# Kernel tuning notes

Measured on AMD Instinct MI355X. Metric: run time of the kernel, lower is better.

## Reference

```python
import jax, jax.numpy as jnp
import numpy as np

DIM = 1024
NUM_HEADS = 16
HEAD_DIM = DIM // NUM_HEADS


def setup_inputs() -> dict:
    key = jax.random.key(0)
    k_x, k_qkv, k_proj, k_pb = jax.random.split(key, 4)
    B, N, C = 4, 2048, DIM
    x = jax.random.normal(k_x, (B, N, C), dtype=jnp.float32)
    # Dense 'qkv': kernel [C, 3C], no bias (qkv_bias=False)
    W_qkv = jax.random.normal(k_qkv, (C, 3 * C), dtype=jnp.float32) * (C ** -0.5)
    # Dense 'proj': kernel [C, C] + bias [C] (proj_bias=True)
    W_proj = jax.random.normal(k_proj, (C, C), dtype=jnp.float32) * (C ** -0.5)
    b_proj = jax.random.normal(k_pb, (C,), dtype=jnp.float32) * 0.01
    return {"x": x, "W_qkv": W_qkv, "W_proj": W_proj, "b_proj": b_proj}


def reference(x, W_qkv, W_proj, b_proj):
    B, N, C = x.shape
    H, D = NUM_HEADS, HEAD_DIM
    scale = D ** -0.5
    qkv = x @ W_qkv  # [B, N, 3C]
    qkv = qkv.reshape(B, N, 3, H, D).transpose(2, 0, 3, 1, 4)  # [3, B, H, N, D]
    q, k, v = qkv[0], qkv[1], qkv[2]
    attn = jnp.einsum('bhnd,bhmd->bhnm', q, k) * scale  # [B, H, N, N]
    attn = jax.nn.softmax(attn, axis=-1)
    out = jnp.einsum('bhnm,bhmd->bhnd', attn, v)  # [B, H, N, D]
    out = out.transpose(0, 2, 1, 3).reshape(B, N, C)
    return out @ W_proj + b_proj
```

## Files before the change

kernel.cpp:

```cpp
#include <hip/hip_runtime.h>
#include <hip/hip_bf16.h>
#include <cstdint>
#include <cstddef>

#define C_DIM 1024
#define N_HEADS 16
#define H_DIM 64
#define N_BATCH 4
#define SEQ_LEN 2048
#define N_BH 64
#define M_ROWS 8192

typedef __attribute__((ext_vector_type(8))) short bf16x8;
typedef __attribute__((ext_vector_type(4))) float f32x4;
typedef __attribute__((ext_vector_type(8))) float f32x8;
typedef __attribute__((ext_vector_type(2))) float f32x2;
typedef __attribute__((ext_vector_type(16))) float f32x16;
typedef __attribute__((ext_vector_type(4))) unsigned short us4;
typedef __attribute__((ext_vector_type(8))) unsigned short us8;
typedef __attribute__((ext_vector_type(4))) float fl4;

__device__ __forceinline__ unsigned short f2bf(float f) {
  union { float f; unsigned u; } v; v.f = f;
  unsigned r = (v.u + 0x7FFFu + ((v.u >> 16) & 1u)) >> 16;
  return (unsigned short)r;
}

__device__ __forceinline__ unsigned pk2(float a, float b) {
  union { __hip_bfloat162 h2; unsigned u; } c;
  c.h2 = __float22bfloat162_rn(float2{a, b});
  return c.u;
}

__device__ __forceinline__ void gload16(const void* g, void* l) {
  __builtin_amdgcn_global_load_lds(
      (const __attribute__((address_space(1))) unsigned int*)g,
      (__attribute__((address_space(3))) unsigned int*)l, 16, 0, 0);
}

__global__ void cast_x_kernel(const float* __restrict__ in,
                              unsigned short* __restrict__ out, int n8) {
  int i = blockIdx.x * blockDim.x + threadIdx.x;
  if (i >= n8) return;
  const fl4* p = reinterpret_cast<const fl4*>(in) + (size_t)i * 2;
  fl4 a = p[0], b = p[1];
  us8 w;
  w[0] = f2bf(a[0]); w[1] = f2bf(a[1]); w[2] = f2bf(a[2]); w[3] = f2bf(a[3]);
  w[4] = f2bf(b[0]); w[5] = f2bf(b[1]); w[6] = f2bf(b[2]); w[7] = f2bf(b[3]);
  *(reinterpret_cast<us8*>(out) + i) = w;
}

__global__ void transpose_cast_kernel(const float* __restrict__ in,
                                      unsigned short* __restrict__ out,
                                      int R, int C) {
  __shared__ float tile[64][65];
  int t = threadIdx.x;
  int tc = blockIdx.x * 64;
  int tr = blockIdx.y * 64;
  int hi = t >> 4, lo = t & 15;
#pragma unroll
  for (int i = 0; i < 4; ++i) {
    int r = i * 16 + hi;
    int c = lo * 4;
    fl4 v = *reinterpret_cast<const fl4*>(&in[(size_t)(tr + r) * C + tc + c]);
    tile[c + 0][r] = v[0]; tile[c + 1][r] = v[1];
    tile[c + 2][r] = v[2]; tile[c + 3][r] = v[3];
  }
  __syncthreads();
#pragma unroll
  for (int i = 0; i < 4; ++i) {
    int c = i * 16 + hi;
    int r = lo * 4;
    us4 w;
    w[0] = f2bf(tile[c][r + 0]); w[1] = f2bf(tile[c][r + 1]);
    w[2] = f2bf(tile[c][r + 2]); w[3] = f2bf(tile[c][r + 3]);
    *reinterpret_cast<us4*>(&out[(size_t)(tc + c) * R + tr + r]) = w;
  }
}

template <int EPI>
__global__ __launch_bounds__(256, 3) void gemm_v2_kernel(
    const unsigned short* __restrict__ A, const unsigned short* __restrict__ Bt,
    unsigned short* __restrict__ outQ, unsigned short* __restrict__ outK,
    unsigned short* __restrict__ outVt, float* __restrict__ outF,
    const float* __restrict__ bias, int K) {
  __shared__ __attribute__((aligned(16))) char lds[3 * 16384];
  const int tid = threadIdx.x;
  const int lane = tid & 63, wave = tid >> 6;
  const int wr = wave >> 1, wn = wave & 1;
  const int brow = blockIdx.y * 128;
  const int bcol = blockIdx.x * 128;
  const int rr = lane & 15, g = lane >> 4;

  const int rbase =
      (rr >> 1) * 128 + (((((rr & 1) << 2) | g) ^ (rr >> 1)) << 4);

  const int s1 = tid + 256;
  const int l0 = tid >> 3, v0 = (tid & 7) ^ (l0 & 7);
  const int l1 = s1 >> 3, v1 = (s1 & 7) ^ (l1 & 7);
  const int m0 = 2 * l0 + (v0 >> 2), g0 = v0 & 3;
  const int m1 = 2 * l1 + (v1 >> 2), g1 = v1 & 3;
  const char* srcA0 = (const char*)(A + (size_t)(brow + m0) * K + g0 * 8);
  const char* srcA1 = (const char*)(A + (size_t)(brow + m1) * K + g1 * 8);
  const char* srcB0 = (const char*)(Bt + (size_t)(bcol + m0) * K + g0 * 8);
  const char* srcB1 = (const char*)(Bt + (size_t)(bcol + m1) * K + g1 * 8);
  const int oA0 = wave * 1024 + (lane & 63) * 16;
  const int oA1 = oA0 + 4096;
  const int oB0 = oA0 + 8192;
  const int oB1 = oA0 + 12288;

  f32x4 acc[4][4];
#pragma unroll
  for (int m = 0; m < 4; ++m)
#pragma unroll
    for (int n = 0; n < 4; ++n) acc[m][n] = (f32x4){0.f, 0.f, 0.f, 0.f};

  const int NT = K >> 5;

#pragma unroll
  for (int pt = 0; pt < 2; ++pt) {
    char* bb = lds + pt * 16384;
    size_t ko = (size_t)pt * 64;
    gload16(srcA0 + ko, bb + oA0);
    gload16(srcA1 + ko, bb + oA1);
    gload16(srcB0 + ko, bb + oB0);
    gload16(srcB1 + ko, bb + oB1);
  }

  int rbuf = 0, nbuf = 2;
  for (int kt = 0; kt < NT; ++kt) {
    if (kt < NT - 1) {
      asm volatile("s_waitcnt vmcnt(4)" ::: "memory");
    } else {
      asm volatile("s_waitcnt vmcnt(0)" ::: "memory");
    }
    __builtin_amdgcn_sched_barrier(0);
    __builtin_amdgcn_s_barrier();
    __builtin_amdgcn_sched_barrier(0);
    if (kt + 2 < NT) {
      char* bb = lds + nbuf * 16384;
      size_t ko = (size_t)(kt + 2) * 64;
      gload16(srcA0 + ko, bb + oA0);
      gload16(srcA1 + ko, bb + oA1);
      gload16(srcB0 + ko, bb + oB0);
      gload16(srcB1 + ko, bb + oB1);
    }
    const char* rb = lds + rbuf * 16384;
    bf16x8 af[4], bf[4];
#pragma unroll
    for (int fm = 0; fm < 4; ++fm)
      af[fm] = *reinterpret_cast<const bf16x8*>(rb + wr * 4096 + fm * 1024 +
                                                rbase);
#pragma unroll
    for (int fn = 0; fn < 4; ++fn)
      bf[fn] = *reinterpret_cast<const bf16x8*>(rb + 8192 + wn * 4096 +
                                                fn * 1024 + rbase);
    asm volatile("s_waitcnt lgkmcnt(0)" ::: "memory");
    __builtin_amdgcn_sched_barrier(0);
    __builtin_amdgcn_s_setprio(1);
#pragma unroll
    for (int fm = 0; fm < 4; ++fm)
#pragma unroll
      for (int fn = 0; fn < 4; ++fn)
        acc[fm][fn] = __builtin_amdgcn_mfma_f32_16x16x32_bf16(
            af[fm], bf[fn], acc[fm][fn], 0, 0, 0);
    __builtin_amdgcn_s_setprio(0);
    rbuf = rbuf == 2 ? 0 : rbuf + 1;
    nbuf = nbuf == 2 ? 0 : nbuf + 1;
  }

  if (EPI == 0) {
    int part = bcol >> 10;
#pragma unroll
    for (int fn = 0; fn < 4; ++fn) {
      int col = (bcol & 1023) + wn * 64 + fn * 16 + rr;
      int h = col >> 6, d = col & 63;
#pragma unroll
      for (int fm = 0; fm < 4; ++fm) {
        int rowb = brow + wr * 64 + fm * 16 + g * 4;
        int b = rowb >> 11, nr = rowb & 2047;
        if (part == 2) {
          us4 w;
#pragma unroll
          for (int r = 0; r < 4; ++r) w[r] = f2bf(acc[fm][fn][r]);
          *reinterpret_cast<us4*>(
              &outVt[((size_t)((b * N_HEADS + h) * H_DIM + d)) * SEQ_LEN +
                     nr]) = w;
        } else {
#pragma unroll
          for (int r = 0; r < 4; ++r) {
            size_t idx =
                ((size_t)((b * N_HEADS + h) * SEQ_LEN + nr + r)) * H_DIM + d;
            float v = acc[fm][fn][r];
            if (part == 0)
              outQ[idx] = f2bf(v * 0.1803368801111837f);
            else
              outK[idx] = f2bf(v);
          }
        }
      }
    }
  } else {
#pragma unroll
    for (int fn = 0; fn < 4; ++fn) {
      int col = bcol + wn * 64 + fn * 16 + rr;
      float bv = bias[col];
#pragma unroll
      for (int fm = 0; fm < 4; ++fm) {
        int rowb = brow + wr * 64 + fm * 16 + g * 4;
#pragma unroll
        for (int r = 0; r < 4; ++r)
          outF[(size_t)(rowb + r) * C_DIM + col] = acc[fm][fn][r] + bv;
      }
    }
  }
}

__global__ __launch_bounds__(256) void attn_kernel(
    const unsigned short* __restrict__ Qs, const unsigned short* __restrict__ Ks,
    const unsigned short* __restrict__ Vts, unsigned short* __restrict__ Oo) {
  __shared__ __attribute__((aligned(16))) char lds[32768];
  const int tid = threadIdx.x;
  const int lane = tid & 63, wave = tid >> 6;
  const int l31 = lane & 31, h5 = lane >> 5;
  int i = blockIdx.x;
  int bh = (i & 7) * 8 + ((i >> 3) & 7);
  int qb = i >> 6;
  const int q0 = qb * 128 + wave * 32;
  const int bb = bh >> 4, hh = bh & 15;

  const unsigned short* Qb = Qs + (size_t)bh * SEQ_LEN * H_DIM;
  const char* Kg = (const char*)(Ks + (size_t)bh * SEQ_LEN * H_DIM);
  const char* Vg = (const char*)(Vts + (size_t)bh * H_DIM * SEQ_LEN);

  bf16x8 qf[4];
#pragma unroll
  for (int ks = 0; ks < 4; ++ks)
    qf[ks] = *reinterpret_cast<const bf16x8*>(
        &Qb[(size_t)(q0 + l31) * H_DIM + ks * 16 + h5 * 8]);

  int kaddr[4];
  int r7 = (l31 & 7) << 4;
#pragma unroll
  for (int ks = 0; ks < 4; ++ks)
    kaddr[ks] = l31 * 128 + ((ks * 32 + h5 * 16) ^ r7);
  int vaddr[2][2][2];
#pragma unroll
  for (int dt = 0; dt < 2; ++dt) {
    int d = dt * 32 + l31;
    int sw = (d & 7) << 4;
#pragma unroll
    for (int s = 0; s < 2; ++s)
#pragma unroll
      for (int m = 0; m < 2; ++m)
        vaddr[dt][s][m] = 8192 + d * 128 + ((s * 64 + m * 32 + h5 * 16) ^ sw);
  }

  const int rowc = lane >> 3;
  const int scb = (((lane & 7) ^ rowc)) * 16;
  const char* gK0 = Kg + (size_t)(wave * 16 + rowc) * 128 + scb;
  const char* gK1 = gK0 + 8 * 128;
  const char* gV0 = Vg + (size_t)(wave * 16 + rowc) * 4096 + scb;
  const char* gV1 = gV0 + 8 * 4096;
  char* lK0 = lds + wave * 2048 + (lane & 63) * 16;
  char* lV0 = lds + 8192 + wave * 2048 + (lane & 63) * 16;

  f32x16 oacc[2];
#pragma unroll
  for (int dt = 0; dt < 2; ++dt)
#pragma unroll
    for (int r = 0; r < 16; ++r) oacc[dt][r] = 0.f;
  float lsum = 0.f;

  f32x16 z16;
#pragma unroll
  for (int r = 0; r < 16; ++r) z16[r] = 0.f;

  {
    gload16(gK0, lK0);
    gload16(gK1, lK0 + 1024);
    gload16(gV0, lV0);
    gload16(gV1, lV0 + 1024);
  }
  __syncthreads();

#pragma unroll 2
  for (int t = 0; t < 32; ++t) {
    int boff = (t & 1) * 16384;
    if (t < 31) {
      int nb = ((t + 1) & 1) * 16384;
      size_t kR = (size_t)(t + 1) * 64 * 128;
      size_t kV = (size_t)(t + 1) * 128;
      gload16(gK0 + kR, lK0 + nb);
      gload16(gK1 + kR, lK0 + nb + 1024);
      gload16(gV0 + kV, lV0 + nb);
      gload16(gV1 + kV, lV0 + nb + 1024);
    }
#pragma unroll
    for (int s = 0; s < 2; ++s) {
      bf16x8 kf[4];
#pragma unroll
      for (int ks = 0; ks < 4; ++ks)
        kf[ks] = *reinterpret_cast<const bf16x8*>(
            lds + boff + kaddr[ks] + s * 4096);
      __builtin_amdgcn_s_setprio(1);
      f32x16 sa = __builtin_amdgcn_mfma_f32_32x32x16_bf16(kf[0], qf[0], z16,
                                                          0, 0, 0);
#pragma unroll
      for (int ks = 1; ks < 4; ++ks)
        sa = __builtin_amdgcn_mfma_f32_32x32x16_bf16(kf[ks], qf[ks], sa, 0, 0, 0);
      __builtin_amdgcn_s_setprio(0);
      f32x16 pv;
#pragma unroll
      for (int r = 0; r < 16; ++r) pv[r] = __builtin_amdgcn_exp2f(sa[r]);
      {
        f32x8 h8 = __builtin_shufflevector(pv, pv, 0, 1, 2, 3, 4, 5, 6, 7) +
                   __builtin_shufflevector(pv, pv, 8, 9, 10, 11, 12, 13, 14, 15);
        f32x4 h4 = __builtin_shufflevector(h8, h8, 0, 1, 2, 3) +
                   __builtin_shufflevector(h8, h8, 4, 5, 6, 7);
        f32x2 h2 = __builtin_shufflevector(h4, h4, 0, 1) +
                   __builtin_shufflevector(h4, h4, 2, 3);
        lsum += h2[0] + h2[1];
      }
      unsigned X0 = pk2(pv[0], pv[1]), X1 = pk2(pv[2], pv[3]);
      unsigned X2 = pk2(pv[4], pv[5]), X3 = pk2(pv[6], pv[7]);
      unsigned X4 = pk2(pv[8], pv[9]), X5 = pk2(pv[10], pv[11]);
      unsigned X6 = pk2(pv[12], pv[13]), X7 = pk2(pv[14], pv[15]);
      asm("v_permlane32_swap_b32 %0, %1" : "+v"(X0), "+v"(X2));
      asm("v_permlane32_swap_b32 %0, %1" : "+v"(X1), "+v"(X3));
      asm("v_permlane32_swap_b32 %0, %1" : "+v"(X4), "+v"(X6));
      asm("v_permlane32_swap_b32 %0, %1" : "+v"(X5), "+v"(X7));
      union { unsigned u[4]; bf16x8 v; } pf0, pf1;
      pf0.u[0] = X0; pf0.u[1] = X1; pf0.u[2] = X2; pf0.u[3] = X3;
      pf1.u[0] = X4; pf1.u[1] = X5; pf1.u[2] = X6; pf1.u[3] = X7;
      bf16x8 vf[2][2];
#pragma unroll
      for (int dt = 0; dt < 2; ++dt)
#pragma unroll
        for (int m = 0; m < 2; ++m)
          vf[dt][m] = *reinterpret_cast<const bf16x8*>(
              lds + boff + vaddr[dt][s][m]);
      __builtin_amdgcn_s_setprio(1);
#pragma unroll
      for (int dt = 0; dt < 2; ++dt) {
        oacc[dt] = __builtin_amdgcn_mfma_f32_32x32x16_bf16(vf[dt][0], pf0.v,
                                                           oacc[dt], 0, 0, 0);
        oacc[dt] = __builtin_amdgcn_mfma_f32_32x32x16_bf16(vf[dt][1], pf1.v,
                                                           oacc[dt], 0, 0, 0);
      }
      __builtin_amdgcn_s_setprio(0);
    }
    __syncthreads();
  }

  lsum += __shfl_xor(lsum, 32);
  float inv = 1.f / lsum;
  int n = q0 + l31;
  unsigned short* orow = Oo + ((size_t)bb * SEQ_LEN + n) * C_DIM + hh * H_DIM;
#pragma unroll
  for (int dt = 0; dt < 2; ++dt)
#pragma unroll
    for (int G = 0; G < 4; ++G) {
      us4 w;
#pragma unroll
      for (int u = 0; u < 4; ++u) w[u] = f2bf(oacc[dt][G * 4 + u] * inv);
      *reinterpret_cast<us4*>(&orow[dt * 32 + G * 8 + h5 * 4]) = w;
    }
}

extern "C" void kernel_launch(void* const* d_in, const int* in_sizes, int n_in,
                              void* d_out, int out_size, void* d_ws,
                              size_t ws_size, hipStream_t stream) {
  const float* x = (const float*)d_in[0];
  const float* Wqkv = (const float*)d_in[1];
  const float* Wproj = (const float*)d_in[2];
  const float* bproj = (const float*)d_in[3];
  float* out = (float*)d_out;

  unsigned short* xbf = (unsigned short*)d_ws;
  unsigned short* Wtqkv = xbf + (size_t)M_ROWS * C_DIM;
  unsigned short* Wtproj = Wtqkv + (size_t)3 * C_DIM * C_DIM;
  unsigned short* Qb = Wtproj + (size_t)C_DIM * C_DIM;
  unsigned short* Kb = Qb + (size_t)N_BH * SEQ_LEN * H_DIM;
  unsigned short* Vtb = Kb + (size_t)N_BH * SEQ_LEN * H_DIM;
  unsigned short* Ob = xbf;

  cast_x_kernel<<<4096, 256, 0, stream>>>(x, xbf, M_ROWS * C_DIM / 8);
  transpose_cast_kernel<<<dim3(48, 16), 256, 0, stream>>>(Wqkv, Wtqkv, C_DIM,
                                                          3 * C_DIM);
  transpose_cast_kernel<<<dim3(16, 16), 256, 0, stream>>>(Wproj, Wtproj, C_DIM,
                                                          C_DIM);
  gemm_v2_kernel<0><<<dim3(24, 64), 256, 0, stream>>>(
      xbf, Wtqkv, Qb, Kb, Vtb, nullptr, nullptr, C_DIM);
  attn_kernel<<<dim3(1024), 256, 0, stream>>>(Qb, Kb, Vtb, Ob);
  gemm_v2_kernel<1><<<dim3(8, 64), 256, 0, stream>>>(
      Ob, Wtproj, nullptr, nullptr, nullptr, out, bproj, C_DIM);
}
```

Before: 208.4 us.

## Store K/V in MFMA fragment order and read them directly from global memory

The QKV GEMM epilogue now writes K and V in a pre-swizzled fragment layout that matches the per-lane operand order of the 32x32x16 MFMA. The attention kernel drops its LDS double buffer and block-wide barriers and loads K and V fragments straight from global (L2-cached) memory with 16-byte per-lane loads. This removes LDS traffic and __syncthreads stalls. In exchange, each wave independently refetches the same K/V data with no cross-wave sharing and no explicit prefetch, so load latency may be exposed. The K epilogue writes also become scattered 2-byte stores.

```diff
diff --git a/kernel.cpp b/kernel.cpp
--- a/kernel.cpp
+++ b/kernel.cpp
@@ -82,7 +82,7 @@
 __global__ __launch_bounds__(256, 3) void gemm_v2_kernel(
     const unsigned short* __restrict__ A, const unsigned short* __restrict__ Bt,
     unsigned short* __restrict__ outQ, unsigned short* __restrict__ outK,
-    unsigned short* __restrict__ outVt, float* __restrict__ outF,
+    unsigned short* __restrict__ outV, float* __restrict__ outF,
     const float* __restrict__ bias, int K) {
   __shared__ __attribute__((aligned(16))) char lds[3 * 16384];
   const int tid = threadIdx.x;
@@ -179,24 +179,31 @@
       for (int fm = 0; fm < 4; ++fm) {
         int rowb = brow + wr * 64 + fm * 16 + g * 4;
         int b = rowb >> 11, nr = rowb & 2047;
-        if (part == 2) {
+        size_t bhbase = (size_t)(b * N_HEADS + h) << 17;
+        if (part == 0) {
+#pragma unroll
+          for (int r = 0; r < 4; ++r)
+            outQ[bhbase + (size_t)(nr + r) * H_DIM + d] =
+                f2bf(acc[fm][fn][r] * 0.1803368801111837f);
+        } else if (part == 1) {
+          int ks = d >> 4, lhi = (d >> 3) & 1, j = d & 7;
+#pragma unroll
+          for (int r = 0; r < 4; ++r) {
+            int n = nr + r;
+            int t = n >> 5, ln = (n & 31) + (lhi << 5);
+            outK[bhbase + (size_t)(((t * 4 + ks) * 64 + ln) * 8 + j)] =
+                f2bf(acc[fm][fn][r]);
+          }
+        } else {
+          int dt = d >> 5, m = (nr >> 4) & 1, t = nr >> 5;
+          int ln = (d & 31) + (((nr >> 3) & 1) << 5);
+          int j0 = nr & 7;
           us4 w;
 #pragma unroll
           for (int r = 0; r < 4; ++r) w[r] = f2bf(acc[fm][fn][r]);
           *reinterpret_cast<us4*>(
-              &outVt[((size_t)((b * N_HEADS + h) * H_DIM + d)) * SEQ_LEN +
-                     nr]) = w;
-        } else {
-#pragma unroll
-          for (int r = 0; r < 4; ++r) {
-            size_t idx =
-                ((size_t)((b * N_HEADS + h) * SEQ_LEN + nr + r)) * H_DIM + d;
-            float v = acc[fm][fn][r];
-            if (part == 0)
-              outQ[idx] = f2bf(v * 0.1803368801111837f);
-            else
-              outK[idx] = f2bf(v);
-          }
+              &outV[bhbase +
+                    (size_t)(((t * 4 + dt * 2 + m) * 64 + ln) * 8 + j0)]) = w;
         }
       }
     }
@@ -217,9 +224,8 @@
 }
 
 __global__ __launch_bounds__(256) void attn_kernel(
-    const unsigned short* __restrict__ Qs, const unsigned short* __restrict__ Ks,
-    const unsigned short* __restrict__ Vts, unsigned short* __restrict__ Oo) {
-  __shared__ __attribute__((aligned(16))) char lds[32768];
+    const unsigned short* __restrict__ Qs, const unsigned short* __restrict__ Kf,
+    const unsigned short* __restrict__ Vf, unsigned short* __restrict__ Oo) {
   const int tid = threadIdx.x;
   const int lane = tid & 63, wave = tid >> 6;
   const int l31 = lane & 31, h5 = lane >> 5;
@@ -229,9 +235,9 @@
   const int q0 = qb * 128 + wave * 32;
   const int bb = bh >> 4, hh = bh & 15;
 
-  const unsigned short* Qb = Qs + (size_t)bh * SEQ_LEN * H_DIM;
-  const char* Kg = (const char*)(Ks + (size_t)bh * SEQ_LEN * H_DIM);
-  const char* Vg = (const char*)(Vts + (size_t)bh * H_DIM * SEQ_LEN);
+  const unsigned short* Qb = Qs + ((size_t)bh << 17);
+  const char* Kb = (const char*)Kf + ((size_t)bh << 18) + lane * 16;
+  const char* Vb = (const char*)Vf + ((size_t)bh << 18) + lane * 16;
 
   bf16x8 qf[4];
 #pragma unroll
@@ -239,32 +245,6 @@
     qf[ks] = *reinterpret_cast<const bf16x8*>(
         &Qb[(size_t)(q0 + l31) * H_DIM + ks * 16 + h5 * 8]);
 
-  int kaddr[4];
-  int r7 = (l31 & 7) << 4;
-#pragma unroll
-  for (int ks = 0; ks < 4; ++ks)
-    kaddr[ks] = l31 * 128 + ((ks * 32 + h5 * 16) ^ r7);
-  int vaddr[2][2][2];
-#pragma unroll
-  for (int dt = 0; dt < 2; ++dt) {
-    int d = dt * 32 + l31;
-    int sw = (d & 7) << 4;
-#pragma unroll
-    for (int s = 0; s < 2; ++s)
-#pragma unroll
-      for (int m = 0; m < 2; ++m)
-        vaddr[dt][s][m] = 8192 + d * 128 + ((s * 64 + m * 32 + h5 * 16) ^ sw);
-  }
-
-  const int rowc = lane >> 3;
-  const int scb = (((lane & 7) ^ rowc)) * 16;
-  const char* gK0 = Kg + (size_t)(wave * 16 + rowc) * 128 + scb;
-  const char* gK1 = gK0 + 8 * 128;
-  const char* gV0 = Vg + (size_t)(wave * 16 + rowc) * 4096 + scb;
-  const char* gV1 = gV0 + 8 * 4096;
-  char* lK0 = lds + wave * 2048 + (lane & 63) * 16;
-  char* lV0 = lds + 8192 + wave * 2048 + (lane & 63) * 16;
-
   f32x16 oacc[2];
 #pragma unroll
   for (int dt = 0; dt < 2; ++dt)
@@ -276,81 +256,60 @@
 #pragma unroll
   for (int r = 0; r < 16; ++r) z16[r] = 0.f;
 
-  {
-    gload16(gK0, lK0);
-    gload16(gK1, lK0 + 1024);
-    gload16(gV0, lV0);
-    gload16(gV1, lV0 + 1024);
-  }
-  __syncthreads();
-
 #pragma unroll 2
-  for (int t = 0; t < 32; ++t) {
-    int boff = (t & 1) * 16384;
-    if (t < 31) {
-      int nb = ((t + 1) & 1) * 16384;
-      size_t kR = (size_t)(t + 1) * 64 * 128;
-      size_t kV = (size_t)(t + 1) * 128;
-      gload16(gK0 + kR, lK0 + nb);
-      gload16(gK1 + kR, lK0 + nb + 1024);
-      gload16(gV0 + kV, lV0 + nb);
-      gload16(gV1 + kV, lV0 + nb + 1024);
-    }
-#pragma unroll
-    for (int s = 0; s < 2; ++s) {
-      bf16x8 kf[4];
-#pragma unroll
-      for (int ks = 0; ks < 4; ++ks)
-        kf[ks] = *reinterpret_cast<const bf16x8*>(
-            lds + boff + kaddr[ks] + s * 4096);
-      __builtin_amdgcn_s_setprio(1);
-      f32x16 sa = __builtin_amdgcn_mfma_f32_32x32x16_bf16(kf[0], qf[0], z16,
-                                                          0, 0, 0);
-#pragma unroll
-      for (int ks = 1; ks < 4; ++ks)
-        sa = __builtin_amdgcn_mfma_f32_32x32x16_bf16(kf[ks], qf[ks], sa, 0, 0, 0);
-      __builtin_amdgcn_s_setprio(0);
-      f32x16 pv;
-#pragma unroll
-      for (int r = 0; r < 16; ++r) pv[r] = __builtin_amdgcn_exp2f(sa[r]);
-      {
-        f32x8 h8 = __builtin_shufflevector(pv, pv, 0, 1, 2, 3, 4, 5, 6, 7) +
-                   __builtin_shufflevector(pv, pv, 8, 9, 10, 11, 12, 13, 14, 15);
-        f32x4 h4 = __builtin_shufflevector(h8, h8, 0, 1, 2, 3) +
-                   __builtin_shufflevector(h8, h8, 4, 5, 6, 7);
-        f32x2 h2 = __builtin_shufflevector(h4, h4, 0, 1) +
-                   __builtin_shufflevector(h4, h4, 2, 3);
-        lsum += h2[0] + h2[1];
-      }
-      unsigned X0 = pk2(pv[0], pv[1]), X1 = pk2(pv[2], pv[3]);
-      unsigned X2 = pk2(pv[4], pv[5]), X3 = pk2(pv[6], pv[7]);
-      unsigned X4 = pk2(pv[8], pv[9]), X5 = pk2(pv[10], pv[11]);
-      unsigned X6 = pk2(pv[12], pv[13]), X7 = pk2(pv[14], pv[15]);
-      asm("v_permlane32_swap_b32 %0, %1" : "+v"(X0), "+v"(X2));
-      asm("v_permlane32_swap_b32 %0, %1" : "+v"(X1), "+v"(X3));
-      asm("v_permlane32_swap_b32 %0, %1" : "+v"(X4), "+v"(X6));
-      asm("v_permlane32_swap_b32 %0, %1" : "+v"(X5), "+v"(X7));
-      union { unsigned u[4]; bf16x8 v; } pf0, pf1;
-      pf0.u[0] = X0; pf0.u[1] = X1; pf0.u[2] = X2; pf0.u[3] = X3;
-      pf1.u[0] = X4; pf1.u[1] = X5; pf1.u[2] = X6; pf1.u[3] = X7;
-      bf16x8 vf[2][2];
-#pragma unroll
-      for (int dt = 0; dt < 2; ++dt)
-#pragma unroll
-        for (int m = 0; m < 2; ++m)
-          vf[dt][m] = *reinterpret_cast<const bf16x8*>(
-              lds + boff + vaddr[dt][s][m]);
-      __builtin_amdgcn_s_setprio(1);
-#pragma unroll
-      for (int dt = 0; dt < 2; ++dt) {
-        oacc[dt] = __builtin_amdgcn_mfma_f32_32x32x16_bf16(vf[dt][0], pf0.v,
-                                                           oacc[dt], 0, 0, 0);
-        oacc[dt] = __builtin_amdgcn_mfma_f32_32x32x16_bf16(vf[dt][1], pf1.v,
-                                                           oacc[dt], 0, 0, 0);
-      }
-      __builtin_amdgcn_s_setprio(0);
-    }
-    __syncthreads();
+  for (int t = 0; t < 64; ++t) {
+    const char* kp = Kb + t * 4096;
+    const char* vp = Vb + t * 4096;
+    bf16x8 kfr[4], vfr[2][2];
+#pragma unroll
+    for (int ks = 0; ks < 4; ++ks)
+      kfr[ks] = *reinterpret_cast<const bf16x8*>(kp + ks * 1024);
+#pragma unroll
+    for (int dt = 0; dt < 2; ++dt)
+#pragma unroll
+      for (int m = 0; m < 2; ++m)
+        vfr[dt][m] =
+            *reinterpret_cast<const bf16x8*>(vp + dt * 2048 + m * 1024);
+
+    __builtin_amdgcn_s_setprio(1);
+    f32x16 sa =
+        __builtin_amdgcn_mfma_f32_32x32x16_bf16(kfr[0], qf[0], z16, 0, 0, 0);
+#pragma unroll
+    for (int ks = 1; ks < 4; ++ks)
+      sa = __builtin_amdgcn_mfma_f32_32x32x16_bf16(kfr[ks], qf[ks], sa, 0, 0, 0);
+    __builtin_amdgcn_s_setprio(0);
+    f32x16 pv;
+#pragma unroll
+    for (int r = 0; r < 16; ++r) pv[r] = __builtin_amdgcn_exp2f(sa[r]);
+    {
+      f32x8 h8 = __builtin_shufflevector(pv, pv, 0, 1, 2, 3, 4, 5, 6, 7) +
+                 __builtin_shufflevector(pv, pv, 8, 9, 10, 11, 12, 13, 14, 15);
+      f32x4 h4 = __builtin_shufflevector(h8, h8, 0, 1, 2, 3) +
+                 __builtin_shufflevector(h8, h8, 4, 5, 6, 7);
+      f32x2 h2 = __builtin_shufflevector(h4, h4, 0, 1) +
+                 __builtin_shufflevector(h4, h4, 2, 3);
+      lsum += h2[0] + h2[1];
+    }
+    unsigned X0 = pk2(pv[0], pv[1]), X1 = pk2(pv[2], pv[3]);
+    unsigned X2 = pk2(pv[4], pv[5]), X3 = pk2(pv[6], pv[7]);
+    unsigned X4 = pk2(pv[8], pv[9]), X5 = pk2(pv[10], pv[11]);
+    unsigned X6 = pk2(pv[12], pv[13]), X7 = pk2(pv[14], pv[15]);
+    asm("v_permlane32_swap_b32 %0, %1" : "+v"(X0), "+v"(X2));
+    asm("v_permlane32_swap_b32 %0, %1" : "+v"(X1), "+v"(X3));
+    asm("v_permlane32_swap_b32 %0, %1" : "+v"(X4), "+v"(X6));
+    asm("v_permlane32_swap_b32 %0, %1" : "+v"(X5), "+v"(X7));
+    union { unsigned u[4]; bf16x8 v; } pf0, pf1;
+    pf0.u[0] = X0; pf0.u[1] = X1; pf0.u[2] = X2; pf0.u[3] = X3;
+    pf1.u[0] = X4; pf1.u[1] = X5; pf1.u[2] = X6; pf1.u[3] = X7;
+    __builtin_amdgcn_s_setprio(1);
+#pragma unroll
+    for (int dt = 0; dt < 2; ++dt) {
+      oacc[dt] = __builtin_amdgcn_mfma_f32_32x32x16_bf16(vfr[dt][0], pf0.v,
+                                                         oacc[dt], 0, 0, 0);
+      oacc[dt] = __builtin_amdgcn_mfma_f32_32x32x16_bf16(vfr[dt][1], pf1.v,
+                                                         oacc[dt], 0, 0, 0);
+    }
+    __builtin_amdgcn_s_setprio(0);
   }
 
   lsum += __shfl_xor(lsum, 32);
@@ -381,8 +340,8 @@
   unsigned short* Wtqkv = xbf + (size_t)M_ROWS * C_DIM;
   unsigned short* Wtproj = Wtqkv + (size_t)3 * C_DIM * C_DIM;
   unsigned short* Qb = Wtproj + (size_t)C_DIM * C_DIM;
-  unsigned short* Kb = Qb + (size_t)N_BH * SEQ_LEN * H_DIM;
-  unsigned short* Vtb = Kb + (size_t)N_BH * SEQ_LEN * H_DIM;
+  unsigned short* Kbf = Qb + (size_t)N_BH * SEQ_LEN * H_DIM;
+  unsigned short* Vbf = Kbf + (size_t)N_BH * SEQ_LEN * H_DIM;
   unsigned short* Ob = xbf;
 
   cast_x_kernel<<<4096, 256, 0, stream>>>(x, xbf, M_ROWS * C_DIM / 8);
@@ -391,8 +350,8 @@
   transpose_cast_kernel<<<dim3(16, 16), 256, 0, stream>>>(Wproj, Wtproj, C_DIM,
                                                           C_DIM);
   gemm_v2_kernel<0><<<dim3(24, 64), 256, 0, stream>>>(
-      xbf, Wtqkv, Qb, Kb, Vtb, nullptr, nullptr, C_DIM);
-  attn_kernel<<<dim3(1024), 256, 0, stream>>>(Qb, Kb, Vtb, Ob);
+      xbf, Wtqkv, Qb, Kbf, Vbf, nullptr, nullptr, C_DIM);
+  attn_kernel<<<dim3(1024), 256, 0, stream>>>(Qb, Kbf, Vbf, Ob);
   gemm_v2_kernel<1><<<dim3(8, 64), 256, 0, stream>>>(
       Ob, Wtproj, nullptr, nullptr, nullptr, out, bproj, C_DIM);
 }
```

Result: faster. 203.0 us (-2.6%).
